# Performance work log

Measured on AMD Instinct MI355X. Metric: run time of the kernel, lower is better.

The kernel has to match this reference:

```python
import jax, jax.numpy as jnp
import numpy as np


def setup_inputs() -> dict:
    key = jax.random.key(0)
    k1, k2 = jax.random.split(key)
    img = jax.random.normal(k1, (4, 96, 256, 256), dtype=jnp.float32)
    light = jax.random.normal(k2, (4, 96, 256, 256), dtype=jnp.float32)
    return {"img": img, "light": light}


def reference(img, light):
    B, C, H, W = img.shape
    F = C // 3
    # NCHW -> NHWC -> [B,H,W,F,3]
    im = img.transpose(0, 2, 3, 1).reshape(B, H, W, F, 3)
    lt = light.transpose(0, 2, 3, 1).reshape(B, H, W, F, 3)
    # per-light intensity magnitude: [B,H,W,F,1]
    I = jnp.linalg.norm(im, axis=-1, keepdims=True)
    # L^T I : [B,H,W,3,1]
    LtI = jnp.einsum('bhwfc,bhwfo->bhwco', lt, I)
    # L^T L : [B,H,W,3,3]
    LtL = jnp.einsum('bhwfc,bhwfd->bhwcd', lt, lt)
    Linv = jnp.linalg.inv(LtL)
    # normal estimate: [B,H,W,3]
    N = jnp.einsum('bhwcd,bhwdo->bhwco', Linv, LtI)[..., 0]
    N = N / (jnp.linalg.norm(N, axis=-1, keepdims=True) + 1e-10)
    # NHWC -> NCHW
    return N.transpose(0, 3, 1, 2)
```

## Files before the change

### kernel.cpp

```cpp
#include <hip/hip_runtime.h>


constexpr int FLIGHTS = 32;
constexpr int QROW    = 16384;
constexpr int CH      = 96;

__device__ __forceinline__ float fc(const float4 v, int j) {
    return j == 0 ? v.x : j == 1 ? v.y : j == 2 ? v.z : v.w;
}
__device__ __forceinline__ void setc(float4& v, int j, float x) {
    if (j == 0) v.x = x; else if (j == 1) v.y = x; else if (j == 2) v.z = x; else v.w = x;
}

__global__ __launch_bounds__(256) void LS_44160853737780_kernel(
    const float4* __restrict__ img,
    const float4* __restrict__ light,
    float4* __restrict__ out)
{
    int q = blockIdx.x * blockDim.x + threadIdx.x;
    int b = q >> 14;
    int p = q & 16383;

    const float4* ib = img   + (size_t)(b * CH) * QROW + p;
    const float4* lb = light + (size_t)(b * CH) * QROW + p;

    float A00[4] = {0,0,0,0}, A01[4] = {0,0,0,0}, A02[4] = {0,0,0,0},
          A11[4] = {0,0,0,0}, A12[4] = {0,0,0,0}, A22[4] = {0,0,0,0},
          r0[4]  = {0,0,0,0}, r1[4]  = {0,0,0,0}, r2[4]  = {0,0,0,0};

    #pragma unroll 4
    for (int f = 0; f < FLIGHTS; ++f) {
        float4 ix = ib[(3 * f + 0) * QROW];
        float4 iy = ib[(3 * f + 1) * QROW];
        float4 iz = ib[(3 * f + 2) * QROW];
        float4 lx = lb[(3 * f + 0) * QROW];
        float4 ly = lb[(3 * f + 1) * QROW];
        float4 lz = lb[(3 * f + 2) * QROW];
        #pragma unroll
        for (int j = 0; j < 4; ++j) {
            float x = fc(ix, j), y = fc(iy, j), z = fc(iz, j);
            float I = sqrtf(x * x + y * y + z * z);
            float a = fc(lx, j), c = fc(ly, j), d = fc(lz, j);
            A00[j] += a * a; A01[j] += a * c; A02[j] += a * d;
            A11[j] += c * c; A12[j] += c * d; A22[j] += d * d;
            r0[j]  += a * I; r1[j]  += c * I; r2[j]  += d * I;
        }
    }

    float4 o0, o1, o2;
    #pragma unroll
    for (int j = 0; j < 4; ++j) {
        float a00 = A00[j], a01 = A01[j], a02 = A02[j],
              a11 = A11[j], a12 = A12[j], a22 = A22[j];
        float c00 = a11 * a22 - a12 * a12;
        float c01 = a02 * a12 - a01 * a22;
        float c02 = a01 * a12 - a02 * a11;
        float c11 = a00 * a22 - a02 * a02;
        float c12 = a01 * a02 - a00 * a12;
        float c22 = a00 * a11 - a01 * a01;
        float det = a00 * c00 + a01 * c01 + a02 * c02;
        float inv = 1.0f / det;
        float n0 = (c00 * r0[j] + c01 * r1[j] + c02 * r2[j]) * inv;
        float n1 = (c01 * r0[j] + c11 * r1[j] + c12 * r2[j]) * inv;
        float n2 = (c02 * r0[j] + c12 * r1[j] + c22 * r2[j]) * inv;
        float nn = sqrtf(n0 * n0 + n1 * n1 + n2 * n2);
        float s  = 1.0f / (nn + 1e-10f);
        setc(o0, j, n0 * s);
        setc(o1, j, n1 * s);
        setc(o2, j, n2 * s);
    }

    float4* ob = out + (size_t)(b * 3) * QROW + p;
    ob[0]        = o0;
    ob[QROW]     = o1;
    ob[2 * QROW] = o2;
}

extern "C" void kernel_launch(void* const* d_in, const int* in_sizes, int n_in,
                              void* d_out, int out_size, void* d_ws, size_t ws_size,
                              hipStream_t stream) {
    const float4* img   = (const float4*)d_in[0];
    const float4* light = (const float4*)d_in[1];
    float4* out = (float4*)d_out;
    LS_44160853737780_kernel<<<dim3(256), dim3(256), 0, stream>>>(img, light, out);
}
```

Before: 209.4 us.

## Split light loop across four lanes per pixel with shuffle reduction

Each group of four threads now handles one float4 pixel quad, each thread accumulating 8 of the 32 lights, and the normal-equation sums are combined with xor shuffles. The grid grows fourfold, raising the number of in-flight loads to better saturate memory bandwidth. The cost is redundant solve computation in every lane, shuffle overhead, and less contiguous per-instruction access across channel planes.

```diff
diff --git a/kernel.cpp b/kernel.cpp
--- a/kernel.cpp
+++ b/kernel.cpp
@@ -1,9 +1,8 @@
 #include <hip/hip_runtime.h>
 
 
-constexpr int FLIGHTS = 32;
-constexpr int QROW    = 16384;
-constexpr int CH      = 96;
+constexpr int QROW = 16384;
+constexpr int CH   = 96;
 
 __device__ __forceinline__ float fc(const float4 v, int j) {
     return j == 0 ? v.x : j == 1 ? v.y : j == 2 ? v.z : v.w;
@@ -12,38 +11,64 @@
     if (j == 0) v.x = x; else if (j == 1) v.y = x; else if (j == 2) v.z = x; else v.w = x;
 }
 
-__global__ __launch_bounds__(256) void LS_44160853737780_kernel(
+__global__ __launch_bounds__(256, 4) void LS_44160853737780_kernel(
     const float4* __restrict__ img,
     const float4* __restrict__ light,
     float4* __restrict__ out)
 {
-    int q = blockIdx.x * blockDim.x + threadIdx.x;
-    int b = q >> 14;
-    int p = q & 16383;
+    int t   = blockIdx.x * blockDim.x + threadIdx.x;
+    int q   = t >> 2;
+    int sub = t & 3;
+    int b   = q >> 14;
+    int p   = q & 16383;
 
-    const float4* ib = img   + (size_t)(b * CH) * QROW + p;
-    const float4* lb = light + (size_t)(b * CH) * QROW + p;
+    const float4* ib = img   + (size_t)(b * CH + sub * 24) * QROW + p;
+    const float4* lb = light + (size_t)(b * CH + sub * 24) * QROW + p;
 
     float A00[4] = {0,0,0,0}, A01[4] = {0,0,0,0}, A02[4] = {0,0,0,0},
           A11[4] = {0,0,0,0}, A12[4] = {0,0,0,0}, A22[4] = {0,0,0,0},
           r0[4]  = {0,0,0,0}, r1[4]  = {0,0,0,0}, r2[4]  = {0,0,0,0};
 
-    #pragma unroll 4
-    for (int f = 0; f < FLIGHTS; ++f) {
-        float4 ix = ib[(3 * f + 0) * QROW];
-        float4 iy = ib[(3 * f + 1) * QROW];
-        float4 iz = ib[(3 * f + 2) * QROW];
-        float4 lx = lb[(3 * f + 0) * QROW];
-        float4 ly = lb[(3 * f + 1) * QROW];
-        float4 lz = lb[(3 * f + 2) * QROW];
+    #pragma unroll
+    for (int f = 0; f < 8; f += 2) {
+        float4 i0x = ib[(3*f+0)*QROW], i0y = ib[(3*f+1)*QROW], i0z = ib[(3*f+2)*QROW];
+        float4 i1x = ib[(3*f+3)*QROW], i1y = ib[(3*f+4)*QROW], i1z = ib[(3*f+5)*QROW];
+        float4 l0x = lb[(3*f+0)*QROW], l0y = lb[(3*f+1)*QROW], l0z = lb[(3*f+2)*QROW];
+        float4 l1x = lb[(3*f+3)*QROW], l1y = lb[(3*f+4)*QROW], l1z = lb[(3*f+5)*QROW];
         #pragma unroll
         for (int j = 0; j < 4; ++j) {
-            float x = fc(ix, j), y = fc(iy, j), z = fc(iz, j);
-            float I = sqrtf(x * x + y * y + z * z);
-            float a = fc(lx, j), c = fc(ly, j), d = fc(lz, j);
-            A00[j] += a * a; A01[j] += a * c; A02[j] += a * d;
-            A11[j] += c * c; A12[j] += c * d; A22[j] += d * d;
-            r0[j]  += a * I; r1[j]  += c * I; r2[j]  += d * I;
+            {
+                float x = fc(i0x,j), y = fc(i0y,j), z = fc(i0z,j);
+                float I = sqrtf(x*x + y*y + z*z);
+                float a = fc(l0x,j), c = fc(l0y,j), d = fc(l0z,j);
+                A00[j] += a*a; A01[j] += a*c; A02[j] += a*d;
+                A11[j] += c*c; A12[j] += c*d; A22[j] += d*d;
+                r0[j]  += a*I; r1[j]  += c*I; r2[j]  += d*I;
+            }
+            {
+                float x = fc(i1x,j), y = fc(i1y,j), z = fc(i1z,j);
+                float I = sqrtf(x*x + y*y + z*z);
+                float a = fc(l1x,j), c = fc(l1y,j), d = fc(l1z,j);
+                A00[j] += a*a; A01[j] += a*c; A02[j] += a*d;
+                A11[j] += c*c; A12[j] += c*d; A22[j] += d*d;
+                r0[j]  += a*I; r1[j]  += c*I; r2[j]  += d*I;
+            }
+        }
+    }
+
+    #pragma unroll
+    for (int m = 1; m <= 2; m <<= 1) {
+        #pragma unroll
+        for (int j = 0; j < 4; ++j) {
+            A00[j] += __shfl_xor(A00[j], m);
+            A01[j] += __shfl_xor(A01[j], m);
+            A02[j] += __shfl_xor(A02[j], m);
+            A11[j] += __shfl_xor(A11[j], m);
+            A12[j] += __shfl_xor(A12[j], m);
+            A22[j] += __shfl_xor(A22[j], m);
+            r0[j]  += __shfl_xor(r0[j],  m);
+            r1[j]  += __shfl_xor(r1[j],  m);
+            r2[j]  += __shfl_xor(r2[j],  m);
         }
     }
 
@@ -52,28 +77,28 @@
     for (int j = 0; j < 4; ++j) {
         float a00 = A00[j], a01 = A01[j], a02 = A02[j],
               a11 = A11[j], a12 = A12[j], a22 = A22[j];
-        float c00 = a11 * a22 - a12 * a12;
-        float c01 = a02 * a12 - a01 * a22;
-        float c02 = a01 * a12 - a02 * a11;
-        float c11 = a00 * a22 - a02 * a02;
-        float c12 = a01 * a02 - a00 * a12;
-        float c22 = a00 * a11 - a01 * a01;
-        float det = a00 * c00 + a01 * c01 + a02 * c02;
+        float c00 = a11*a22 - a12*a12;
+        float c01 = a02*a12 - a01*a22;
+        float c02 = a01*a12 - a02*a11;
+        float c11 = a00*a22 - a02*a02;
+        float c12 = a01*a02 - a00*a12;
+        float c22 = a00*a11 - a01*a01;
+        float det = a00*c00 + a01*c01 + a02*c02;
         float inv = 1.0f / det;
-        float n0 = (c00 * r0[j] + c01 * r1[j] + c02 * r2[j]) * inv;
-        float n1 = (c01 * r0[j] + c11 * r1[j] + c12 * r2[j]) * inv;
-        float n2 = (c02 * r0[j] + c12 * r1[j] + c22 * r2[j]) * inv;
-        float nn = sqrtf(n0 * n0 + n1 * n1 + n2 * n2);
+        float n0 = (c00*r0[j] + c01*r1[j] + c02*r2[j]) * inv;
+        float n1 = (c01*r0[j] + c11*r1[j] + c12*r2[j]) * inv;
+        float n2 = (c02*r0[j] + c12*r1[j] + c22*r2[j]) * inv;
+        float nn = sqrtf(n0*n0 + n1*n1 + n2*n2);
         float s  = 1.0f / (nn + 1e-10f);
-        setc(o0, j, n0 * s);
-        setc(o1, j, n1 * s);
-        setc(o2, j, n2 * s);
+        setc(o0, j, n0*s);
+        setc(o1, j, n1*s);
+        setc(o2, j, n2*s);
     }
 
-    float4* ob = out + (size_t)(b * 3) * QROW + p;
-    ob[0]        = o0;
-    ob[QROW]     = o1;
-    ob[2 * QROW] = o2;
+    if (sub < 3) {
+        float4 v = (sub == 0) ? o0 : (sub == 1) ? o1 : o2;
+        out[(size_t)(b * 3 + sub) * QROW + p] = v;
+    }
 }
 
 extern "C" void kernel_launch(void* const* d_in, const int* in_sizes, int n_in,
@@ -82,5 +107,5 @@
     const float4* img   = (const float4*)d_in[0];
     const float4* light = (const float4*)d_in[1];
     float4* out = (float4*)d_out;
-    LS_44160853737780_kernel<<<dim3(256), dim3(256), 0, stream>>>(img, light, out);
+    LS_44160853737780_kernel<<<dim3(1024), dim3(256), 0, stream>>>(img, light, out);
 }
```

After: 213.6 us. 2.0% more time.
